# Performance work log

Measured on AMD Instinct MI355X. Metric: run time of the kernel, lower is better.

## Reference

```python
import jax, jax.numpy as jnp
import numpy as np

EPS = 1e-5
GROUPS = 32

def octree_conv(x, neigh, W, b):
    # x: [N, Cin], neigh: [N, 27] (-1 => empty neighbor), W: [27, Cin, Cout]
    N = x.shape[0]
    xp = jnp.concatenate([x, jnp.zeros((1, x.shape[1]), x.dtype)], axis=0)  # zero row for empties
    idx = jnp.where(neigh < 0, N, neigh)
    g = xp[idx]                                # [N, 27, Cin] gathered neighbor features
    return jnp.einsum('nkc,kcd->nd', g, W) + b

def octree_group_norm(x, weight, bias, groups=GROUPS):
    # Normalize each group over all non-empty nodes and the channels in the group.
    N, C = x.shape
    xg = x.reshape(N, groups, C // groups)
    mean = jnp.mean(xg, axis=(0, 2), keepdims=True)
    var = jnp.mean(jnp.square(xg - mean), axis=(0, 2), keepdims=True)
    xn = ((xg - mean) * jax.lax.rsqrt(var + EPS)).reshape(N, C)
    return xn * weight + bias

def setup_inputs() -> dict:
    key = jax.random.key(0)
    ks = jax.random.split(key, 8)
    N, Cin, Cmid, Cout, K = 50000, 128, 128, 32, 27
    data = jax.random.normal(ks[0], (N, Cin), dtype=jnp.float32)
    neigh = jax.random.randint(ks[1], (N, K), 0, N, dtype=jnp.int64)
    W1 = jax.random.normal(ks[2], (K, Cin, Cmid), dtype=jnp.float32) * (1.0 / np.sqrt(K * Cin))
    b1 = jnp.zeros((Cmid,), dtype=jnp.float32)
    gn_w = jnp.ones((Cmid,), dtype=jnp.float32)
    gn_b = jnp.zeros((Cmid,), dtype=jnp.float32)
    W2 = jax.random.normal(ks[3], (K, Cmid, Cout), dtype=jnp.float32) * (1.0 / np.sqrt(K * Cmid))
    b2 = jnp.zeros((Cout,), dtype=jnp.float32)
    return {"data": data, "neigh": neigh, "W1": W1, "b1": b1,
            "gn_w": gn_w, "gn_b": gn_b, "W2": W2, "b2": b2}

def reference(data, neigh, W1, b1, gn_w, gn_b, W2, b2):
    x = octree_conv(data, neigh, W1, b1)          # conv1: in -> mid
    x = octree_group_norm(x, gn_w, gn_b)          # GroupNorm over nodes per group
    x = jax.nn.silu(x)                            # SiLU
    x = octree_conv(x, neigh, W2, b2)             # conv2: mid -> out
    return x
```

## Files before the change

kernel.cpp:

```cpp
#include <hip/hip_runtime.h>
#include <stdint.h>

#define N_NODES 50000
#define CIN 128
#define CMID 128
#define COUT 32
#define KNB 27
#define EPSV 1e-5f

typedef __attribute__((ext_vector_type(4))) float f4v;
typedef __attribute__((ext_vector_type(8))) short s8v;
typedef __attribute__((ext_vector_type(4))) short s4v;

__device__ __forceinline__ unsigned short f2bf(float f) {
  union { float f; uint32_t u; } v; v.f = f;
  return (unsigned short)((v.u + 0x7FFFu + ((v.u >> 16) & 1u)) >> 16);
}

__device__ __forceinline__ f4v mfma16(s8v a, s8v b, f4v c) {
  return __builtin_amdgcn_mfma_f32_16x16x32_bf16(a, b, c, 0, 0, 0);
}

__device__ __forceinline__ void gload_lds16(const void* g, void* lds) {
  __builtin_amdgcn_global_load_lds(
      (const __attribute__((address_space(1))) uint32_t*)(uintptr_t)g,
      (__attribute__((address_space(3))) uint32_t*)(uint32_t)(uintptr_t)lds,
      16, 0, 0);
}

__global__ void k_flag(const int* __restrict__ neigh_raw, int* __restrict__ flag) {
  if (threadIdx.x == 0) {
    int ok = 1;
    for (int i = 0; i < 16; ++i) {
      int hi = neigh_raw[2 * i + 1];
      if (hi != 0 && hi != -1) ok = 0;
    }
    *flag = ok;
  }
}

__global__ __launch_bounds__(256) void k_transpose(
    const void* __restrict__ neigh, int* __restrict__ neighT,
    const int* __restrict__ flag)
{
  __shared__ int tT[KNB][257];
  const int r0 = blockIdx.x * 256;
  const bool is64 = (*flag != 0);
  const int tid = threadIdx.x;
  for (int e = tid; e < 256 * KNB; e += 256) {
    int r = e / KNB, k = e - r * KNB;
    if (r0 + r < N_NODES) {
      long long v = is64 ? ((const long long*)neigh)[(size_t)r0 * KNB + e]
                         : (long long)((const int*)neigh)[(size_t)r0 * KNB + e];
      tT[k][r] = (v < 0) ? N_NODES : (int)v;
    }
  }
  __syncthreads();
  for (int e = tid; e < KNB * 256; e += 256) {
    int k = e >> 8, r = e & 255;
    if (r0 + r < N_NODES) neighT[(size_t)k * N_NODES + r0 + r] = tT[k][r];
  }
}

__global__ __launch_bounds__(256) void k_prep(
    const float* __restrict__ data, const float* __restrict__ W1,
    const float* __restrict__ W2,
    short* __restrict__ xb, short* __restrict__ wt1f, short* __restrict__ wt2f,
    float* __restrict__ gsums)
{
  const int TOT0 = (N_NODES + 1) * (CIN / 4);
  const int TOTW1 = KNB * 4 * 8 * 64;
  const int TOTW2 = KNB * 4 * 2 * 64;
  int gtid = blockIdx.x * 256 + threadIdx.x;
  int stride = gridDim.x * 256;
  for (int i = gtid; i < TOT0 + TOTW1 + TOTW2; i += stride) {
    if (i < TOT0) {
      int row = i >> 5, c4 = i & 31;
      s4v o = {};
      if (row < N_NODES) {
        f4v v = *(const f4v*)(data + (size_t)row * CIN + c4 * 4);
        o[0] = (short)f2bf(v[0]); o[1] = (short)f2bf(v[1]);
        o[2] = (short)f2bf(v[2]); o[3] = (short)f2bf(v[3]);
      }
      *(s4v*)(xb + (size_t)row * CIN + c4 * 4) = o;
    } else if (i < TOT0 + TOTW1) {
      int c = i - TOT0;
      int k = c >> 11, rem = c & 2047;
      int kc = rem >> 9, rem2 = rem & 511;
      int n = rem2 >> 6, l = rem2 & 63;
      int cin0 = kc * 32 + (l >> 4) * 8, cout = n * 16 + (l & 15);
      s8v o;
#pragma unroll
      for (int e = 0; e < 8; ++e)
        o[e] = (short)f2bf(W1[(size_t)k * (CIN * CMID) + (cin0 + e) * CMID + cout]);
      *(s8v*)(wt1f + (size_t)c * 8) = o;
    } else {
      int c = i - TOT0 - TOTW1;
      int k = c >> 9, rem = c & 511;
      int kc = rem >> 7, rem2 = rem & 127;
      int n = rem2 >> 6, l = rem2 & 63;
      int cin0 = kc * 32 + (l >> 4) * 8, cout = n * 16 + (l & 15);
      s8v o;
#pragma unroll
      for (int e = 0; e < 8; ++e)
        o[e] = (short)f2bf(W2[(size_t)k * (CMID * COUT) + (cin0 + e) * COUT + cout]);
      *(s8v*)(wt2f + (size_t)c * 8) = o;
    }
  }
  if (gtid < 64) gsums[gtid] = 0.0f;
}

__global__ __launch_bounds__(256, 2) void k_conv1(
    const short* __restrict__ xb, const int* __restrict__ neighT,
    const short* __restrict__ wt1f, short* __restrict__ x1p)
{
  __shared__ short Bs[2][8192];
  __shared__ short As[4][2][2048];
  const int tid = threadIdx.x;
  const int l = tid & 63, w = tid >> 6;
  const int bx = blockIdx.x;
  const int kh = (bx >= 391) ? 1 : 0;
  const int rb = kh ? bx - 391 : bx;
  const int rw = rb * 128 + w * 32;
  const int k0 = kh ? 13 : 0, k1 = kh ? 27 : 13;
  const int lr = l & 15, lho = l >> 4;
  const int l8 = l >> 3, ls = l & 7;

  f4v acc[2][8] = {};
  int idx[4], idxn[4];
  s8v ga[4];

  auto loadIdx = [&](int* id, int k) {
#pragma unroll
    for (int q = 0; q < 4; ++q) {
      int r = rw + q * 8 + l8; if (r >= N_NODES) r = N_NODES - 1;
      id[q] = neighT[(size_t)k * N_NODES + r];
    }
  };
  auto stageB = [&](int buf, int k, int h) {
    const short* src = wt1f + ((size_t)(k * 4 + h * 2) * 8) * 512 + l * 8;
#pragma unroll
    for (int j = 0; j < 4; ++j)
      gload_lds16(src + (w * 4 + j) * 512, &Bs[buf][(w * 4 + j) * 512]);
  };
  auto gatherA = [&](const int* id, int h) {
#pragma unroll
    for (int q = 0; q < 4; ++q)
      ga[q] = *(const s8v*)(xb + (size_t)id[q] * CIN + h * 64 + ls * 8);
  };
  auto writeA = [&](int buf) {
#pragma unroll
    for (int q = 0; q < 4; ++q)
      *(s8v*)&As[w][buf][(q * 8 + l8) * 64 + ((ls ^ l8) * 8)] = ga[q];
  };
  auto compute = [&](int cb) {
#pragma unroll
    for (int kc = 0; kc < 2; ++kc) {
      s8v af[2];
#pragma unroll
      for (int rg = 0; rg < 2; ++rg) {
        int row = rg * 16 + lr;
        af[rg] = *(const s8v*)&As[w][cb][row * 64 + (((kc * 4 + lho) ^ (lr & 7)) * 8)];
      }
#pragma unroll
      for (int n = 0; n < 8; ++n) {
        s8v bf = *(const s8v*)&Bs[cb][(kc * 8 + n) * 512 + l * 8];
        acc[0][n] = mfma16(af[0], bf, acc[0][n]);
        acc[1][n] = mfma16(af[1], bf, acc[1][n]);
      }
    }
  };

  loadIdx(idx, k0);
  stageB(0, k0, 0);
  gatherA(idx, 0);
  __syncthreads();
  writeA(0);

  int cur = 0;
  for (int k = k0; k < k1; ++k) {
    const bool more = (k + 1 < k1);
    stageB(cur ^ 1, k, 1);
    gatherA(idx, 1);
    if (more) loadIdx(idxn, k + 1);
    compute(cur);
    __syncthreads();
    writeA(cur ^ 1);
    cur ^= 1;
    if (more) { stageB(cur ^ 1, k + 1, 0); gatherA(idxn, 0); }
    compute(cur);
    __syncthreads();
    if (more) {
      writeA(cur ^ 1);
#pragma unroll
      for (int q = 0; q < 4; ++q) idx[q] = idxn[q];
    }
    cur ^= 1;
  }

  short* xp = x1p + (size_t)kh * N_NODES * CMID;
#pragma unroll
  for (int rg = 0; rg < 2; ++rg) {
#pragma unroll
    for (int j = 0; j < 4; ++j) {
      int grow = rw + rg * 16 + lho * 4 + j;
      if (grow < N_NODES) {
#pragma unroll
        for (int n = 0; n < 8; ++n)
          xp[(size_t)grow * CMID + n * 16 + lr] = (short)f2bf(acc[rg][n][j]);
      }
    }
  }
}

__global__ __launch_bounds__(256) void k_sum(
    const short* __restrict__ x1p, const float* __restrict__ b1,
    float* __restrict__ gsums)
{
  __shared__ float sh[64];
  const int tid = threadIdx.x;
  if (tid < 64) sh[tid] = 0.0f;
  __syncthreads();
  const int g = tid & 31;
  const short* p0 = x1p;
  const short* p1 = x1p + (size_t)N_NODES * CMID;
  f4v bv = *(const f4v*)(b1 + g * 4);
  float s = 0.f, ss = 0.f;
  for (int r = blockIdx.x * 8 + (tid >> 5); r < N_NODES; r += gridDim.x * 8) {
    s4v v0 = *(const s4v*)(p0 + (size_t)r * CMID + g * 4);
    s4v v1 = *(const s4v*)(p1 + (size_t)r * CMID + g * 4);
#pragma unroll
    for (int e = 0; e < 4; ++e) {
      float x = __uint_as_float(((uint32_t)(uint16_t)v0[e]) << 16) +
                __uint_as_float(((uint32_t)(uint16_t)v1[e]) << 16) + bv[e];
      s += x; ss += x * x;
    }
  }
  s += __shfl_xor(s, 32); ss += __shfl_xor(ss, 32);
  if ((tid & 32) == 0) { atomicAdd(&sh[g], s); atomicAdd(&sh[32 + g], ss); }
  __syncthreads();
  if (tid < 64) atomicAdd(&gsums[tid], sh[tid]);
}

__global__ __launch_bounds__(256) void k_gnsilu(
    const short* __restrict__ x1p, const float* __restrict__ b1,
    const float* __restrict__ gsums, const float* __restrict__ gn_w,
    const float* __restrict__ gn_b, short* __restrict__ xnb)
{
  const float invc = 1.0f / (N_NODES * 4.0f);
  const short* p0 = x1p;
  const short* p1 = x1p + (size_t)N_NODES * CMID;
  int gtid = blockIdx.x * 256 + threadIdx.x;
  int stride = gridDim.x * 256;
  const int TOT = (N_NODES + 1) * (CMID / 4);
  for (int i = gtid; i < TOT; i += stride) {
    int row = i >> 5, g = i & 31;
    s4v o = {};
    if (row < N_NODES) {
      float mean = gsums[g] * invc;
      float var = gsums[32 + g] * invc - mean * mean;
      float rs = rsqrtf(var + EPSV);
      s4v v0 = *(const s4v*)(p0 + (size_t)row * CMID + g * 4);
      s4v v1 = *(const s4v*)(p1 + (size_t)row * CMID + g * 4);
      f4v bv = *(const f4v*)(b1 + g * 4);
      f4v wv = *(const f4v*)(gn_w + g * 4);
      f4v gv = *(const f4v*)(gn_b + g * 4);
#pragma unroll
      for (int e = 0; e < 4; ++e) {
        float x = __uint_as_float(((uint32_t)(uint16_t)v0[e]) << 16) +
                  __uint_as_float(((uint32_t)(uint16_t)v1[e]) << 16) + bv[e];
        float xn = (x - mean) * rs * wv[e] + gv[e];
        float y = xn / (1.0f + __expf(-xn));
        o[e] = (short)f2bf(y);
      }
    }
    *(s4v*)(xnb + (size_t)row * CMID + g * 4) = o;
  }
}

__global__ __launch_bounds__(256, 4) void k_conv2(
    const short* __restrict__ xnb, const int* __restrict__ neighT,
    const short* __restrict__ wt2f, float* __restrict__ x2p)
{
  __shared__ short Bs[2][2048];
  __shared__ short As[4][2][2048];
  const int tid = threadIdx.x;
  const int l = tid & 63, w = tid >> 6;
  const int bx = blockIdx.x;
  const int kh = (bx >= 391) ? 1 : 0;
  const int rb = kh ? bx - 391 : bx;
  const int rw = rb * 128 + w * 32;
  const int k0 = kh ? 13 : 0, k1 = kh ? 27 : 13;
  const int lr = l & 15, lho = l >> 4;
  const int l8 = l >> 3, ls = l & 7;

  f4v acc[2][2] = {};
  int idx[4], idxn[4];
  s8v ga[4];

  auto loadIdx = [&](int* id, int k) {
#pragma unroll
    for (int q = 0; q < 4; ++q) {
      int r = rw + q * 8 + l8; if (r >= N_NODES) r = N_NODES - 1;
      id[q] = neighT[(size_t)k * N_NODES + r];
    }
  };
  auto stageB = [&](int buf, int k, int h) {
    const short* src = wt2f + ((size_t)(k * 4 + h * 2) * 2) * 512 + l * 8;
    gload_lds16(src + w * 512, &Bs[buf][w * 512]);
  };
  auto gatherA = [&](const int* id, int h) {
#pragma unroll
    for (int q = 0; q < 4; ++q)
      ga[q] = *(const s8v*)(xnb + (size_t)id[q] * CMID + h * 64 + ls * 8);
  };
  auto writeA = [&](int buf) {
#pragma unroll
    for (int q = 0; q < 4; ++q)
      *(s8v*)&As[w][buf][(q * 8 + l8) * 64 + ((ls ^ l8) * 8)] = ga[q];
  };
  auto compute = [&](int cb) {
#pragma unroll
    for (int kc = 0; kc < 2; ++kc) {
      s8v af[2];
#pragma unroll
      for (int rg = 0; rg < 2; ++rg) {
        int row = rg * 16 + lr;
        af[rg] = *(const s8v*)&As[w][cb][row * 64 + (((kc * 4 + lho) ^ (lr & 7)) * 8)];
      }
#pragma unroll
      for (int n = 0; n < 2; ++n) {
        s8v bf = *(const s8v*)&Bs[cb][(kc * 2 + n) * 512 + l * 8];
        acc[0][n] = mfma16(af[0], bf, acc[0][n]);
        acc[1][n] = mfma16(af[1], bf, acc[1][n]);
      }
    }
  };

  loadIdx(idx, k0);
  stageB(0, k0, 0);
  gatherA(idx, 0);
  __syncthreads();
  writeA(0);

  int cur = 0;
  for (int k = k0; k < k1; ++k) {
    const bool more = (k + 1 < k1);
    stageB(cur ^ 1, k, 1);
    gatherA(idx, 1);
    if (more) loadIdx(idxn, k + 1);
    compute(cur);
    __syncthreads();
    writeA(cur ^ 1);
    cur ^= 1;
    if (more) { stageB(cur ^ 1, k + 1, 0); gatherA(idxn, 0); }
    compute(cur);
    __syncthreads();
    if (more) {
      writeA(cur ^ 1);
#pragma unroll
      for (int q = 0; q < 4; ++q) idx[q] = idxn[q];
    }
    cur ^= 1;
  }

  float* xp = x2p + (size_t)kh * N_NODES * COUT;
#pragma unroll
  for (int rg = 0; rg < 2; ++rg) {
#pragma unroll
    for (int j = 0; j < 4; ++j) {
      int grow = rw + rg * 16 + lho * 4 + j;
      if (grow < N_NODES) {
#pragma unroll
        for (int n = 0; n < 2; ++n)
          xp[(size_t)grow * COUT + n * 16 + lr] = acc[rg][n][j];
      }
    }
  }
}

__global__ __launch_bounds__(256) void k_fin(
    const float* __restrict__ x2p, const float* __restrict__ b2,
    float* __restrict__ out)
{
  int i = blockIdx.x * 256 + threadIdx.x;
  const int TOT = N_NODES * COUT / 4;
  if (i < TOT) {
    int c4 = i & 7;
    f4v a = *(const f4v*)(x2p + (size_t)i * 4);
    f4v b = *(const f4v*)(x2p + (size_t)N_NODES * COUT + (size_t)i * 4);
    f4v bias = *(const f4v*)(b2 + c4 * 4);
    f4v o = a + b + bias;
    *(f4v*)(out + (size_t)i * 4) = o;
  }
}

extern "C" void kernel_launch(void* const* d_in, const int* in_sizes, int n_in,
                              void* d_out, int out_size, void* d_ws, size_t ws_size,
                              hipStream_t stream) {
  const float* data = (const float*)d_in[0];
  const void* neigh = d_in[1];
  const float* W1   = (const float*)d_in[2];
  const float* b1   = (const float*)d_in[3];
  const float* gn_w = (const float*)d_in[4];
  const float* gn_b = (const float*)d_in[5];
  const float* W2   = (const float*)d_in[6];
  const float* b2   = (const float*)d_in[7];

  char* p = (char*)d_ws;
  short* xb   = (short*)p; p += (size_t)(N_NODES + 1) * CIN * 2;
  float* x2p  = (float*)xb;
  short* wt1f = (short*)p; p += (size_t)KNB * CMID * CIN * 2;
  short* wt2f = (short*)p; p += (size_t)KNB * COUT * CMID * 2;
  short* x1p  = (short*)p; p += (size_t)2 * N_NODES * CMID * 2;
  short* xnb  = (short*)p; p += (size_t)(N_NODES + 1) * CMID * 2;
  int*   neighT = (int*)p; p += (size_t)KNB * N_NODES * 4;
  float* gsums = (float*)p;
  int* flag = (int*)(gsums + 64);

  k_flag<<<1, 64, 0, stream>>>((const int*)neigh, flag);
  k_transpose<<<(N_NODES + 255) / 256, 256, 0, stream>>>(neigh, neighT, flag);
  k_prep<<<2048, 256, 0, stream>>>(data, W1, W2, xb, wt1f, wt2f, gsums);
  k_conv1<<<782, 256, 0, stream>>>(xb, neighT, wt1f, x1p);
  k_sum<<<391, 256, 0, stream>>>(x1p, b1, gsums);
  k_gnsilu<<<2048, 256, 0, stream>>>(x1p, b1, gsums, gn_w, gn_b, xnb);
  k_conv2<<<782, 256, 0, stream>>>(xnb, neighT, wt2f, x2p);
  k_fin<<<(N_NODES * COUT / 4 + 255) / 256, 256, 0, stream>>>(x2p, b2, (float*)d_out);
}
```

Baseline: 234.5 us.

## Gather A fragments directly into registers, drop LDS staging for activations

Both conv kernels now load gathered neighbor rows straight into MFMA A-operand registers instead of staging them through a swizzled LDS buffer. The main loop is flattened into a single-stage software pipeline with sched barriers and hand-placed s_waitcnt before a raw s_barrier. conv2 also processes the full 128-channel K slice per step with a larger B buffer, and conv1 raises its occupancy target to 3 blocks. This removes LDS writes/reads and one barrier per half-step, at the cost of more registers and fragile manual vmcnt counts.

```diff
diff --git a/kernel.cpp b/kernel.cpp
--- a/kernel.cpp
+++ b/kernel.cpp
@@ -27,6 +27,8 @@
       (__attribute__((address_space(3))) uint32_t*)(uint32_t)(uintptr_t)lds,
       16, 0, 0);
 }
+
+#define SBAR() __builtin_amdgcn_sched_barrier(0)
 
 __global__ void k_flag(const int* __restrict__ neigh_raw, int* __restrict__ flag) {
   if (threadIdx.x == 0) {
@@ -110,12 +112,11 @@
   if (gtid < 64) gsums[gtid] = 0.0f;
 }
 
-__global__ __launch_bounds__(256, 2) void k_conv1(
+__global__ __launch_bounds__(256, 3) void k_conv1(
     const short* __restrict__ xb, const int* __restrict__ neighT,
     const short* __restrict__ wt1f, short* __restrict__ x1p)
 {
   __shared__ short Bs[2][8192];
-  __shared__ short As[4][2][2048];
   const int tid = threadIdx.x;
   const int l = tid & 63, w = tid >> 6;
   const int bx = blockIdx.x;
@@ -123,78 +124,73 @@
   const int rb = kh ? bx - 391 : bx;
   const int rw = rb * 128 + w * 32;
   const int k0 = kh ? 13 : 0, k1 = kh ? 27 : 13;
+  const int S = 2 * (k1 - k0);
   const int lr = l & 15, lho = l >> 4;
-  const int l8 = l >> 3, ls = l & 7;
+
+  int ra = rw + lr;       if (ra >= N_NODES) ra = N_NODES - 1;
+  int rb2 = rw + 16 + lr; if (rb2 >= N_NODES) rb2 = N_NODES - 1;
 
   f4v acc[2][8] = {};
-  int idx[4], idxn[4];
-  s8v ga[4];
-
-  auto loadIdx = [&](int* id, int k) {
-#pragma unroll
-    for (int q = 0; q < 4; ++q) {
-      int r = rw + q * 8 + l8; if (r >= N_NODES) r = N_NODES - 1;
-      id[q] = neighT[(size_t)k * N_NODES + r];
-    }
-  };
-  auto stageB = [&](int buf, int k, int h) {
-    const short* src = wt1f + ((size_t)(k * 4 + h * 2) * 8) * 512 + l * 8;
+  s8v Ac[2][2], An[2][2];
+  int ia, ib, ia2 = 0, ib2 = 0;
+
+  auto stageB = [&](int buf, int s) {
+    int k = k0 + (s >> 1), h = s & 1;
+    const short* src = wt1f + (size_t)((k * 4 + h * 2) * 8) * 512 + l * 8;
 #pragma unroll
     for (int j = 0; j < 4; ++j)
       gload_lds16(src + (w * 4 + j) * 512, &Bs[buf][(w * 4 + j) * 512]);
   };
-  auto gatherA = [&](const int* id, int h) {
-#pragma unroll
-    for (int q = 0; q < 4; ++q)
-      ga[q] = *(const s8v*)(xb + (size_t)id[q] * CIN + h * 64 + ls * 8);
-  };
-  auto writeA = [&](int buf) {
-#pragma unroll
-    for (int q = 0; q < 4; ++q)
-      *(s8v*)&As[w][buf][(q * 8 + l8) * 64 + ((ls ^ l8) * 8)] = ga[q];
-  };
-  auto compute = [&](int cb) {
+  auto gatherA = [&](s8v A[2][2], int i0, int i1, int h) {
+    const short* p0 = xb + (size_t)i0 * CIN + h * 64 + lho * 8;
+    const short* p1 = xb + (size_t)i1 * CIN + h * 64 + lho * 8;
 #pragma unroll
     for (int kc = 0; kc < 2; ++kc) {
-      s8v af[2];
-#pragma unroll
-      for (int rg = 0; rg < 2; ++rg) {
-        int row = rg * 16 + lr;
-        af[rg] = *(const s8v*)&As[w][cb][row * 64 + (((kc * 4 + lho) ^ (lr & 7)) * 8)];
-      }
+      A[0][kc] = *(const s8v*)(p0 + kc * 32);
+      A[1][kc] = *(const s8v*)(p1 + kc * 32);
+    }
+  };
+  auto compute = [&](int cb, s8v A[2][2]) {
+#pragma unroll
+    for (int kc = 0; kc < 2; ++kc) {
 #pragma unroll
       for (int n = 0; n < 8; ++n) {
         s8v bf = *(const s8v*)&Bs[cb][(kc * 8 + n) * 512 + l * 8];
-        acc[0][n] = mfma16(af[0], bf, acc[0][n]);
-        acc[1][n] = mfma16(af[1], bf, acc[1][n]);
-      }
-    }
-  };
-
-  loadIdx(idx, k0);
-  stageB(0, k0, 0);
-  gatherA(idx, 0);
+        acc[0][n] = mfma16(A[0][kc], bf, acc[0][n]);
+        acc[1][n] = mfma16(A[1][kc], bf, acc[1][n]);
+      }
+    }
+  };
+
+  ia = neighT[(size_t)k0 * N_NODES + ra];
+  ib = neighT[(size_t)k0 * N_NODES + rb2];
+  stageB(0, 0);
+  gatherA(Ac, ia, ib, 0);
   __syncthreads();
-  writeA(0);
 
   int cur = 0;
-  for (int k = k0; k < k1; ++k) {
-    const bool more = (k + 1 < k1);
-    stageB(cur ^ 1, k, 1);
-    gatherA(idx, 1);
-    if (more) loadIdx(idxn, k + 1);
-    compute(cur);
-    __syncthreads();
-    writeA(cur ^ 1);
-    cur ^= 1;
-    if (more) { stageB(cur ^ 1, k + 1, 0); gatherA(idxn, 0); }
-    compute(cur);
-    __syncthreads();
-    if (more) {
-      writeA(cur ^ 1);
-#pragma unroll
-      for (int q = 0; q < 4; ++q) idx[q] = idxn[q];
-    }
+  for (int s = 0; s < S; ++s) {
+    const int h = s & 1, k = k0 + (s >> 1);
+    if (s + 1 < S) stageB(cur ^ 1, s + 1);
+    SBAR();
+    if (h == 0 && k + 1 < k1) {
+      ia2 = neighT[(size_t)(k + 1) * N_NODES + ra];
+      ib2 = neighT[(size_t)(k + 1) * N_NODES + rb2];
+    }
+    SBAR();
+    if (s + 1 < S) {
+      if (h == 0) gatherA(An, ia, ib, 1);
+      else        gatherA(An, ia2, ib2, 0);
+    }
+    SBAR();
+    compute(cur, Ac);
+    asm volatile("s_waitcnt vmcnt(4) lgkmcnt(0)" ::: "memory");
+    SBAR();
+    __builtin_amdgcn_s_barrier();
+    SBAR();
+    if (h == 1) { ia = ia2; ib = ib2; }
+#pragma unroll
+    for (int kc = 0; kc < 2; ++kc) { Ac[0][kc] = An[0][kc]; Ac[1][kc] = An[1][kc]; }
     cur ^= 1;
   }
 
@@ -282,8 +278,7 @@
     const short* __restrict__ xnb, const int* __restrict__ neighT,
     const short* __restrict__ wt2f, float* __restrict__ x2p)
 {
-  __shared__ short Bs[2][2048];
-  __shared__ short As[4][2][2048];
+  __shared__ short Bs[2][4096];
   const int tid = threadIdx.x;
   const int l = tid & 63, w = tid >> 6;
   const int bx = blockIdx.x;
@@ -291,76 +286,73 @@
   const int rb = kh ? bx - 391 : bx;
   const int rw = rb * 128 + w * 32;
   const int k0 = kh ? 13 : 0, k1 = kh ? 27 : 13;
+  const int S = k1 - k0;
   const int lr = l & 15, lho = l >> 4;
-  const int l8 = l >> 3, ls = l & 7;
+
+  int ra = rw + lr;       if (ra >= N_NODES) ra = N_NODES - 1;
+  int rb2 = rw + 16 + lr; if (rb2 >= N_NODES) rb2 = N_NODES - 1;
 
   f4v acc[2][2] = {};
-  int idx[4], idxn[4];
-  s8v ga[4];
-
-  auto loadIdx = [&](int* id, int k) {
-#pragma unroll
-    for (int q = 0; q < 4; ++q) {
-      int r = rw + q * 8 + l8; if (r >= N_NODES) r = N_NODES - 1;
-      id[q] = neighT[(size_t)k * N_NODES + r];
-    }
-  };
-  auto stageB = [&](int buf, int k, int h) {
-    const short* src = wt2f + ((size_t)(k * 4 + h * 2) * 2) * 512 + l * 8;
-    gload_lds16(src + w * 512, &Bs[buf][w * 512]);
-  };
-  auto gatherA = [&](const int* id, int h) {
-#pragma unroll
-    for (int q = 0; q < 4; ++q)
-      ga[q] = *(const s8v*)(xnb + (size_t)id[q] * CMID + h * 64 + ls * 8);
-  };
-  auto writeA = [&](int buf) {
-#pragma unroll
-    for (int q = 0; q < 4; ++q)
-      *(s8v*)&As[w][buf][(q * 8 + l8) * 64 + ((ls ^ l8) * 8)] = ga[q];
-  };
-  auto compute = [&](int cb) {
-#pragma unroll
-    for (int kc = 0; kc < 2; ++kc) {
-      s8v af[2];
-#pragma unroll
-      for (int rg = 0; rg < 2; ++rg) {
-        int row = rg * 16 + lr;
-        af[rg] = *(const s8v*)&As[w][cb][row * 64 + (((kc * 4 + lho) ^ (lr & 7)) * 8)];
-      }
+  s8v Ac[2][4], An[2][4];
+  int ian = 0, ibn = 0, ia2 = 0, ib2 = 0;
+
+  auto stageB = [&](int buf, int k) {
+    const short* src = wt2f + (size_t)(k * 8) * 512 + l * 8;
+#pragma unroll
+    for (int j = 0; j < 2; ++j)
+      gload_lds16(src + (w * 2 + j) * 512, &Bs[buf][(w * 2 + j) * 512]);
+  };
+  auto gatherA = [&](s8v A[2][4], int i0, int i1) {
+    const short* p0 = xnb + (size_t)i0 * CMID + lho * 8;
+    const short* p1 = xnb + (size_t)i1 * CMID + lho * 8;
+#pragma unroll
+    for (int kc = 0; kc < 4; ++kc) {
+      A[0][kc] = *(const s8v*)(p0 + kc * 32);
+      A[1][kc] = *(const s8v*)(p1 + kc * 32);
+    }
+  };
+  auto compute = [&](int cb, s8v A[2][4]) {
+#pragma unroll
+    for (int kc = 0; kc < 4; ++kc) {
 #pragma unroll
       for (int n = 0; n < 2; ++n) {
         s8v bf = *(const s8v*)&Bs[cb][(kc * 2 + n) * 512 + l * 8];
-        acc[0][n] = mfma16(af[0], bf, acc[0][n]);
-        acc[1][n] = mfma16(af[1], bf, acc[1][n]);
-      }
-    }
-  };
-
-  loadIdx(idx, k0);
-  stageB(0, k0, 0);
-  gatherA(idx, 0);
+        acc[0][n] = mfma16(A[0][kc], bf, acc[0][n]);
+        acc[1][n] = mfma16(A[1][kc], bf, acc[1][n]);
+      }
+    }
+  };
+
+  int iac = neighT[(size_t)k0 * N_NODES + ra];
+  int ibc = neighT[(size_t)k0 * N_NODES + rb2];
+  if (S > 1) {
+    ian = neighT[(size_t)(k0 + 1) * N_NODES + ra];
+    ibn = neighT[(size_t)(k0 + 1) * N_NODES + rb2];
+  }
+  stageB(0, k0);
+  gatherA(Ac, iac, ibc);
   __syncthreads();
-  writeA(0);
 
   int cur = 0;
-  for (int k = k0; k < k1; ++k) {
-    const bool more = (k + 1 < k1);
-    stageB(cur ^ 1, k, 1);
-    gatherA(idx, 1);
-    if (more) loadIdx(idxn, k + 1);
-    compute(cur);
-    __syncthreads();
-    writeA(cur ^ 1);
-    cur ^= 1;
-    if (more) { stageB(cur ^ 1, k + 1, 0); gatherA(idxn, 0); }
-    compute(cur);
-    __syncthreads();
-    if (more) {
-      writeA(cur ^ 1);
-#pragma unroll
-      for (int q = 0; q < 4; ++q) idx[q] = idxn[q];
-    }
+  for (int s = 0; s < S; ++s) {
+    const int k = k0 + s;
+    if (s + 1 < S) stageB(cur ^ 1, k + 1);
+    SBAR();
+    if (s + 2 < S) {
+      ia2 = neighT[(size_t)(k + 2) * N_NODES + ra];
+      ib2 = neighT[(size_t)(k + 2) * N_NODES + rb2];
+    }
+    SBAR();
+    if (s + 1 < S) gatherA(An, ian, ibn);
+    SBAR();
+    compute(cur, Ac);
+    asm volatile("s_waitcnt vmcnt(8) lgkmcnt(0)" ::: "memory");
+    SBAR();
+    __builtin_amdgcn_s_barrier();
+    SBAR();
+    ian = ia2; ibn = ib2;
+#pragma unroll
+    for (int kc = 0; kc < 4; ++kc) { Ac[0][kc] = An[0][kc]; Ac[1][kc] = An[1][kc]; }
     cur ^= 1;
   }
 
```

Result: slower. 261.2 us (+11.4%).
